# Kernel tuning notes

Measured on AMD Instinct MI355X. Metric: run time of the kernel, lower is better.

Reference implementation:

```python
import jax, jax.numpy as jnp
import numpy as np
from jax import lax

NB_DIGITS = 2
BASE = 10
NUMS = BASE ** NB_DIGITS            # 100 possible values per number
SUMS = 2 * (NUMS - 1) + 1           # 199 possible sums (circuit roots)
B = 4096                            # logical batch size
N_IMAGES = B * 2 * NB_DIGITS        # 16384 digit images


def setup_inputs() -> dict:
    key = jax.random.key(0)
    ks = jax.random.split(key, 11)
    s = 0.1
    return {
        "images": jax.random.normal(ks[0], (N_IMAGES, 1, 28, 28), jnp.float32),
        "conv1_w": jax.random.normal(ks[1], (6, 1, 5, 5), jnp.float32) * s,
        "conv1_b": jax.random.normal(ks[2], (6,), jnp.float32) * s,
        "conv2_w": jax.random.normal(ks[3], (16, 6, 5, 5), jnp.float32) * s,
        "conv2_b": jax.random.normal(ks[4], (16,), jnp.float32) * s,
        "fc1_w": jax.random.normal(ks[5], (120, 256), jnp.float32) * s,
        "fc1_b": jax.random.normal(ks[6], (120,), jnp.float32) * s,
        "fc2_w": jax.random.normal(ks[7], (84, 120), jnp.float32) * s,
        "fc2_b": jax.random.normal(ks[8], (84,), jnp.float32) * s,
        "fc3_w": jax.random.normal(ks[9], (10, 84), jnp.float32) * s,
        "fc3_b": jax.random.normal(ks[10], (10,), jnp.float32) * s,
    }


def _conv(x, w, b):
    y = lax.conv_general_dilated(x, w, (1, 1), 'VALID',
                                 dimension_numbers=('NCHW', 'OIHW', 'NCHW'))
    return y + b[None, :, None, None]


def _maxpool2(x):
    return lax.reduce_window(x, -jnp.inf, lax.max, (1, 1, 2, 2), (1, 1, 2, 2), 'VALID')


def _lenet(x, c1w, c1b, c2w, c2b, f1w, f1b, f2w, f2b, f3w, f3b):
    x = jax.nn.relu(_maxpool2(_conv(x, c1w, c1b)))   # [N,6,12,12]
    x = jax.nn.relu(_maxpool2(_conv(x, c2w, c2b)))   # [N,16,4,4]
    x = x.reshape(-1, 16 * 4 * 4)
    x = jax.nn.relu(x @ f1w.T + f1b)
    x = jax.nn.relu(x @ f2w.T + f2b)
    x = x @ f3w.T + f3b
    return jax.nn.log_softmax(x, axis=-1)            # [N,10]


def _circuit(lp):
    # lp: [B, 2*NB_DIGITS, 10] per-digit log-probs.
    # Vars layout from get_circuit: positions 0..NB_DIGITS-1 = n1 digits (MSB first),
    # positions NB_DIGITS..2*NB_DIGITS-1 = n2 digits. Neg-literal weights are 0 in
    # log space (the `zeros` arg), so each model's weight = sum of digit log-probs;
    # OR over models = logsumexp grouped by n1+n2.
    d = jnp.arange(NUMS)
    hi, lo = d // BASE, d % BASE
    lp1 = lp[:, 0, hi] + lp[:, 1, lo]                # [B, NUMS] log P(n1=k)
    lp2 = lp[:, 2, hi] + lp[:, 3, lo]                # [B, NUMS] log P(n2=k)
    M = (lp1[:, :, None] + lp2[:, None, :]).reshape(lp.shape[0], -1)  # [B, NUMS^2]
    seg = (jnp.arange(NUMS)[:, None] + jnp.arange(NUMS)[None, :]).reshape(-1)
    Mf = M.T                                          # [NUMS^2, B]
    m = jax.ops.segment_max(Mf, seg, num_segments=SUMS)              # [SUMS, B]
    ssum = jax.ops.segment_sum(jnp.exp(Mf - m[seg]), seg, num_segments=SUMS)
    return (jnp.log(ssum) + m).T                      # [B, SUMS] log P(sum=s)


def reference(images, conv1_w, conv1_b, conv2_w, conv2_b,
              fc1_w, fc1_b, fc2_w, fc2_b, fc3_w, fc3_b):
    logp = _lenet(images, conv1_w, conv1_b, conv2_w, conv2_b,
                  fc1_w, fc1_b, fc2_w, fc2_b, fc3_w, fc3_b)   # [N_IMAGES,10]
    lp = logp.reshape(B, 2 * NB_DIGITS, BASE)
    return _circuit(lp)
```

## Files before the change

### kernel.cpp

```cpp
#include <hip/hip_runtime.h>
#include <hip/hip_bf16.h>
#include <math.h>

#define SUMS 199
#define NBLK 1024

typedef __attribute__((ext_vector_type(8))) short short8;
typedef __attribute__((ext_vector_type(4))) float float4v;

union Frag8 { short8 v; unsigned u[4]; uint4 q; };

static __device__ inline unsigned pk_bf16(float a, float b) {
    __hip_bfloat162 h = __float22bfloat162_rn(make_float2(a, b));
    union { __hip_bfloat162 h; unsigned u; } c; c.h = h; return c.u;
}

__global__ __launch_bounds__(256) void convert_weights(
    const float* __restrict__ f1w, const float* __restrict__ f2w,
    const float* __restrict__ f3w, const float* __restrict__ c1w,
    const float* __restrict__ c2w, uint4* __restrict__ ws)
{
    const int g = blockIdx.x * 256 + threadIdx.x;
    if (g >= 6400) return;
    float v[8];
    if (g < 5824) {
        const float* W; int O, K, ld, nt, s, l;
        if (g < 4096)      { W = f1w; O = 120; K = 256; ld = 256; nt = g >> 9; s = (g >> 6) & 7; l = g & 63; }
        else if (g < 5632) { const int f = g - 4096; W = f2w; O = 84; K = 120; ld = 120; nt = f >> 8; s = (f >> 6) & 3; l = f & 63; }
        else               { const int f = g - 5632; W = f3w; O = 10; K = 84;  ld = 84;  nt = 0; s = f >> 6; l = f & 63; }
        const int o = nt * 16 + (l & 15);
        #pragma unroll
        for (int j = 0; j < 8; ++j) {
            const int k = 32 * s + 8 * (l >> 4) + j;
            v[j] = (o < O && k < K) ? W[o * ld + k] : 0.f;
        }
    } else if (g < 6336) {
        const int f = g - 5824, s = f >> 6, l = f & 63;
        const int c = l & 15, h = l >> 4;
        #pragma unroll
        for (int jp = 0; jp < 4; ++jp) {
            const int D = 16 * s + 4 * h + jp;
            const int ky = D / 24, rem = D % 24, kx = rem >> 2, icp = rem & 3;
            const bool ok = (ky < 5 && kx < 5);
            v[2 * jp]     = (ok && 2 * icp < 6)     ? c2w[c * 150 + (2 * icp) * 25 + ky * 5 + kx]     : 0.f;
            v[2 * jp + 1] = (ok && 2 * icp + 1 < 6) ? c2w[c * 150 + (2 * icp + 1) * 25 + ky * 5 + kx] : 0.f;
        }
    } else {
        const int l = (g - 6336) & 63;
        const int c = l & 15, h = l >> 4;
        const int oc = c >> 1, xs = c & 1;
        #pragma unroll
        for (int j = 0; j < 8; ++j) {
            const int p = h * 4 + (j >> 1);
            float w = 0.f;
            if (p < 15 && c < 12) {
                const int ky = p / 3, kx = 2 * (p % 3) + (j & 1) - xs;
                if (kx >= 0 && kx < 5) w = c1w[oc * 25 + ky * 5 + kx];
            }
            v[j] = w;
        }
    }
    uint4 r;
    r.x = pk_bf16(v[0], v[1]); r.y = pk_bf16(v[2], v[3]);
    r.z = pk_bf16(v[4], v[5]); r.w = pk_bf16(v[6], v[7]);
    ws[g] = r;
}

__global__ __launch_bounds__(256) void lenet_circuit_kernel(
    const float* __restrict__ images,
    const float* __restrict__ c1b, const float* __restrict__ c2b,
    const float* __restrict__ f1b, const float* __restrict__ f2b,
    const float* __restrict__ f3b, const uint4* __restrict__ wsb,
    float* __restrict__ out)
{
    __shared__ __align__(16) unsigned char s_mem[39712];
    unsigned*       imgu = (unsigned*)s_mem;
    unsigned short* p1s  = (unsigned short*)(s_mem + 12576);
    const uint4*    p1u4 = (const uint4*)(s_mem + 12576);
    unsigned*       A1d  = (unsigned*)(s_mem + 31264);
    const uint4*    A1q  = (const uint4*)(s_mem + 31264);

    const int t = threadIdx.x, bid = blockIdx.x;
    const int lane = t & 63, wav = t >> 6;
    const int c = lane & 15, h = lane >> 4;
    const uint4 z4 = {0u, 0u, 0u, 0u};

    {
        uint4* pz = (uint4*)(s_mem + 12576);
        for (int i = t; i < 1168; i += 256) pz[i] = z4;
    }
    Frag8 a1; a1.q = wsb[6336 + lane];
    Frag8 w2[8];
    #pragma unroll
    for (int s = 0; s < 8; ++s) w2[s].q = wsb[5824 + s * 64 + lane];
    int koff[8];
    #pragma unroll
    for (int s = 0; s < 8; ++s) {
        const int D0 = 16 * s + 4 * h;
        koff[s] = (D0 / 24) * 12 + ((D0 % 24) >> 2);
    }
    int pd[4];
    #pragma unroll
    for (int q = 0; q < 4; ++q) {
        const int p = 4 * h + q;
        pd[q] = (p < 15) ? (p / 3) * 14 + (p % 3) : 0;
    }
    float bias0 = 0.f, bias1 = 0.f;
    if (h < 3) { bias0 = c1b[2 * h]; bias1 = c1b[2 * h + 1]; }
    const float b2v = c2b[c];

    for (int pass = 0; pass < 2; ++pass) {
        {
            const float4* g = (const float4*)(images + (size_t)bid * 12544 + pass * 6272);
            for (int i = t; i < 1568; i += 256) {
                const float4 v = g[i];
                const int im = i / 196, j = i % 196;
                imgu[im * 393 + 2 * j]     = pk_bf16(v.x, v.y);
                imgu[im * 393 + 2 * j + 1] = pk_bf16(v.z, v.w);
            }
        }
        __syncthreads();

        {
            const int n = c, img = n >> 1;
            const int imb = img * 393 + (n & 1) * 14;
            for (int qy = wav * 3; qy < wav * 3 + 3; ++qy) {
                #pragma unroll
                for (int qx = 0; qx < 12; ++qx) {
                    const int base = imb + qy * 28 + qx;
                    Frag8 bf;
                    #pragma unroll
                    for (int q = 0; q < 4; ++q) bf.u[q] = imgu[base + pd[q]];
                    float4v acc = {0.f, 0.f, 0.f, 0.f};
                    acc = __builtin_amdgcn_mfma_f32_16x16x32_bf16(a1.v, bf.v, acc, 0, 0, 0);
                    float v0 = fmaxf(acc[0], acc[1]);
                    float v1 = fmaxf(acc[2], acc[3]);
                    v0 = fmaxf(v0, __shfl_xor(v0, 1));
                    v1 = fmaxf(v1, __shfl_xor(v1, 1));
                    if ((n & 1) == 0 && h < 3) {
                        const unsigned pkv = pk_bf16(fmaxf(v0 + bias0, 0.f),
                                                     fmaxf(v1 + bias1, 0.f));
                        *(unsigned*)&p1s[img * 1152 + qy * 96 + qx * 8 + 2 * h] = pkv;
                    }
                }
            }
        }
        __syncthreads();

        {
            const int pxl = (c & 1) + 2 * ((c >> 2) & 1);
            const int pyl = ((c >> 1) & 1) + 2 * ((c >> 3) & 1);
            #pragma unroll
            for (int ii = 0; ii < 2; ++ii) {
                const int i0 = 2 * wav + ii;
                #pragma unroll
                for (int mt = 0; mt < 4; ++mt) {
                    const int px = pxl + 4 * (mt & 1), py = pyl + 4 * (mt >> 1);
                    const int base = i0 * 144 + py * 12 + px;
                    float4v acc = {0.f, 0.f, 0.f, 0.f};
                    #pragma unroll
                    for (int s = 0; s < 8; ++s) {
                        Frag8 af; af.q = p1u4[base + koff[s]];
                        acc = __builtin_amdgcn_mfma_f32_16x16x32_bf16(af.v, w2[s].v, acc, 0, 0, 0);
                    }
                    const float p = fmaxf(fmaxf(acc[0], acc[1]), fmaxf(acc[2], acc[3]));
                    float v = fmaxf(p + b2v, 0.f);
                    const float vp = __shfl_xor(v, 16);
                    if ((h & 1) == 0) {
                        const int qy = (h >> 1) + 2 * (mt >> 1);
                        A1d[(pass * 8 + i0) * 132 + c * 8 + qy * 2 + (mt & 1)] = pk_bf16(v, vp);
                    }
                }
            }
        }
    }
    __syncthreads();

    {
        unsigned* A2d = (unsigned*)s_mem;
        if (t < 64) A2d[(t >> 2) * 68 + 60 + (t & 3)] = 0u;
        float4v acc0 = {0.f, 0.f, 0.f, 0.f}, acc1 = acc0;
        const int nt0 = 2 * wav;
        #pragma unroll
        for (int s = 0; s < 8; ++s) {
            Frag8 af; af.q = A1q[c * 33 + 4 * s + h];
            Frag8 b0; b0.q = wsb[(nt0 * 8 + s) * 64 + lane];
            Frag8 b1; b1.q = wsb[((nt0 + 1) * 8 + s) * 64 + lane];
            acc0 = __builtin_amdgcn_mfma_f32_16x16x32_bf16(af.v, b0.v, acc0, 0, 0, 0);
            acc1 = __builtin_amdgcn_mfma_f32_16x16x32_bf16(af.v, b1.v, acc1, 0, 0, 0);
        }
        #pragma unroll
        for (int ntl = 0; ntl < 2; ++ntl) {
            const int o = 32 * wav + 16 * ntl + c;
            const float bias = (o < 120) ? f1b[o] : 0.f;
            #pragma unroll
            for (int r = 0; r < 4; ++r) {
                float v = fmaxf((ntl ? acc1[r] : acc0[r]) + bias, 0.f);
                const float vp = __shfl_xor(v, 1);
                if ((c & 1) == 0 && o < 120)
                    A2d[(4 * h + r) * 68 + (o >> 1)] = pk_bf16(v, vp);
            }
        }
    }
    __syncthreads();

    {
        unsigned* A3d = (unsigned*)(s_mem + 4352);
        if (t < 96) A3d[(t / 6) * 52 + 42 + (t % 6)] = 0u;
        if (wav < 3) {
            const uint4* A2q = (const uint4*)s_mem;
            float4v acc0 = {0.f, 0.f, 0.f, 0.f}, acc1 = acc0;
            const int nt0 = 2 * wav;
            #pragma unroll
            for (int s = 0; s < 4; ++s) {
                Frag8 af; af.q = A2q[c * 17 + 4 * s + h];
                Frag8 b0; b0.q = wsb[4096 + (nt0 * 4 + s) * 64 + lane];
                Frag8 b1; b1.q = wsb[4096 + ((nt0 + 1) * 4 + s) * 64 + lane];
                acc0 = __builtin_amdgcn_mfma_f32_16x16x32_bf16(af.v, b0.v, acc0, 0, 0, 0);
                acc1 = __builtin_amdgcn_mfma_f32_16x16x32_bf16(af.v, b1.v, acc1, 0, 0, 0);
            }
            #pragma unroll
            for (int ntl = 0; ntl < 2; ++ntl) {
                const int o = 32 * wav + 16 * ntl + c;
                const float bias = (o < 84) ? f2b[o] : 0.f;
                #pragma unroll
                for (int r = 0; r < 4; ++r) {
                    float v = fmaxf((ntl ? acc1[r] : acc0[r]) + bias, 0.f);
                    const float vp = __shfl_xor(v, 1);
                    if ((c & 1) == 0 && o < 84)
                        A3d[(4 * h + r) * 52 + (o >> 1)] = pk_bf16(v, vp);
                }
            }
        }
    }
    __syncthreads();

    float* lgf = (float*)(s_mem + 7680);
    float* e1f = (float*)(s_mem + 8448);
    float* e2f = (float*)(s_mem + 10048);

    if (wav == 0) {
        const uint4* A3q = (const uint4*)(s_mem + 4352);
        float4v acc = {0.f, 0.f, 0.f, 0.f};
        #pragma unroll
        for (int s = 0; s < 3; ++s) {
            Frag8 af; af.q = A3q[c * 13 + 4 * s + h];
            Frag8 b; b.q = wsb[5632 + s * 64 + lane];
            acc = __builtin_amdgcn_mfma_f32_16x16x32_bf16(af.v, b.v, acc, 0, 0, 0);
        }
        if (c < 10) {
            const float bias = f3b[c];
            #pragma unroll
            for (int r = 0; r < 4; ++r) lgf[(4 * h + r) * 12 + c] = acc[r] + bias;
        }
    }
    __syncthreads();

    if (t < 16) {
        float* lp = lgf + t * 12;
        float mx = -INFINITY;
        #pragma unroll
        for (int i = 0; i < 10; ++i) mx = fmaxf(mx, lp[i]);
        float sum = 0.f;
        #pragma unroll
        for (int i = 0; i < 10; ++i) sum += expf(lp[i] - mx);
        const float lse = mx + logf(sum);
        #pragma unroll
        for (int i = 0; i < 10; ++i) lp[i] -= lse;
    }
    __syncthreads();

    for (int idx = t; idx < 800; idx += 256) {
        const int be = idx / 200, r = idx % 200;
        const float* lp = lgf + 4 * be * 12;
        if (r < 100) e1f[be * 100 + r] = expf(lp[r / 10] + lp[12 + r % 10]);
        else { const int k = r - 100; e2f[be * 100 + k] = expf(lp[24 + k / 10] + lp[36 + k % 10]); }
    }
    __syncthreads();

    for (int pid = t; pid < 400; pid += 256) {
        const int be = pid / 100, sp = pid % 100;
        const float* E1 = e1f + be * 100;
        const float* E2 = e2f + be * 100;
        float* ob = out + ((size_t)bid * 4 + be) * SUMS;
        float s1 = 0.f;
        for (int i = 0; i <= sp; ++i) s1 += E1[i] * E2[sp - i];
        ob[sp] = logf(s1);
        if (sp >= 1) {
            float s2 = 0.f;
            for (int i = sp; i <= 99; ++i) s2 += E1[i] * E2[sp + 99 - i];
            ob[sp + 99] = logf(s2);
        }
    }
}

extern "C" void kernel_launch(void* const* d_in, const int* in_sizes, int n_in,
                              void* d_out, int out_size, void* d_ws, size_t ws_size,
                              hipStream_t stream) {
    const float* images = (const float*)d_in[0];
    const float* c1w = (const float*)d_in[1];
    const float* c1b = (const float*)d_in[2];
    const float* c2w = (const float*)d_in[3];
    const float* c2b = (const float*)d_in[4];
    const float* f1w = (const float*)d_in[5];
    const float* f1b = (const float*)d_in[6];
    const float* f2w = (const float*)d_in[7];
    const float* f2b = (const float*)d_in[8];
    const float* f3w = (const float*)d_in[9];
    const float* f3b = (const float*)d_in[10];
    float* out = (float*)d_out;

    convert_weights<<<25, 256, 0, stream>>>(f1w, f2w, f3w, c1w, c2w, (uint4*)d_ws);
    lenet_circuit_kernel<<<NBLK, 256, 0, stream>>>(
        images, c1b, c2b, f1b, f2b, f3b, (const uint4*)d_ws, out);
}
```

Before: 151.4 us.

## Double block to 512 threads and vectorize circuit convolution with phase-shifted float4 buffers

The fused kernel now launches 512 threads (8 waves) per block, and every stage's work split is redistributed so each wave handles fewer conv tiles, images or FC output tiles. The final sum-convolution stores zero-padded, phase-shifted copies of E1 and a reversed E2 so each output is a contiguous aligned float4 dot product. One thread now computes each output pair, so more threads do work at once and the shared-memory loads are vectorized. The cost is higher register pressure from launch_bounds(512,8), more LDS writes for the four phase copies, and some idle waves in the FC3 stage.

Result: slower. 260.0 us (+71.8%).

```diff
diff --git a/kernel.cpp b/kernel.cpp
--- a/kernel.cpp
+++ b/kernel.cpp
@@ -66,7 +66,7 @@
     ws[g] = r;
 }
 
-__global__ __launch_bounds__(256) void lenet_circuit_kernel(
+__global__ __launch_bounds__(512, 8) void lenet_circuit_kernel(
     const float* __restrict__ images,
     const float* __restrict__ c1b, const float* __restrict__ c2b,
     const float* __restrict__ f1b, const float* __restrict__ f2b,
@@ -79,6 +79,8 @@
     const uint4*    p1u4 = (const uint4*)(s_mem + 12576);
     unsigned*       A1d  = (unsigned*)(s_mem + 31264);
     const uint4*    A1q  = (const uint4*)(s_mem + 31264);
+    float*          E1Pf = (float*)(s_mem + 12576);
+    float*          E2Rf = (float*)(s_mem + 19232);
 
     const int t = threadIdx.x, bid = blockIdx.x;
     const int lane = t & 63, wav = t >> 6;
@@ -87,7 +89,7 @@
 
     {
         uint4* pz = (uint4*)(s_mem + 12576);
-        for (int i = t; i < 1168; i += 256) pz[i] = z4;
+        for (int i = t; i < 1168; i += 512) pz[i] = z4;
     }
     Frag8 a1; a1.q = wsb[6336 + lane];
     Frag8 w2[8];
@@ -112,7 +114,7 @@
     for (int pass = 0; pass < 2; ++pass) {
         {
             const float4* g = (const float4*)(images + (size_t)bid * 12544 + pass * 6272);
-            for (int i = t; i < 1568; i += 256) {
+            for (int i = t; i < 1568; i += 512) {
                 const float4 v = g[i];
                 const int im = i / 196, j = i % 196;
                 imgu[im * 393 + 2 * j]     = pk_bf16(v.x, v.y);
@@ -124,82 +126,73 @@
         {
             const int n = c, img = n >> 1;
             const int imb = img * 393 + (n & 1) * 14;
-            for (int qy = wav * 3; qy < wav * 3 + 3; ++qy) {
+            for (int task = wav * 18; task < wav * 18 + 18; ++task) {
+                const int qy = task / 12, qx = task % 12;
+                const int base = imb + qy * 28 + qx;
+                Frag8 bf;
                 #pragma unroll
-                for (int qx = 0; qx < 12; ++qx) {
-                    const int base = imb + qy * 28 + qx;
-                    Frag8 bf;
-                    #pragma unroll
-                    for (int q = 0; q < 4; ++q) bf.u[q] = imgu[base + pd[q]];
-                    float4v acc = {0.f, 0.f, 0.f, 0.f};
-                    acc = __builtin_amdgcn_mfma_f32_16x16x32_bf16(a1.v, bf.v, acc, 0, 0, 0);
-                    float v0 = fmaxf(acc[0], acc[1]);
-                    float v1 = fmaxf(acc[2], acc[3]);
-                    v0 = fmaxf(v0, __shfl_xor(v0, 1));
-                    v1 = fmaxf(v1, __shfl_xor(v1, 1));
-                    if ((n & 1) == 0 && h < 3) {
-                        const unsigned pkv = pk_bf16(fmaxf(v0 + bias0, 0.f),
-                                                     fmaxf(v1 + bias1, 0.f));
-                        *(unsigned*)&p1s[img * 1152 + qy * 96 + qx * 8 + 2 * h] = pkv;
-                    }
+                for (int q = 0; q < 4; ++q) bf.u[q] = imgu[base + pd[q]];
+                float4v acc = {0.f, 0.f, 0.f, 0.f};
+                acc = __builtin_amdgcn_mfma_f32_16x16x32_bf16(a1.v, bf.v, acc, 0, 0, 0);
+                float v0 = fmaxf(acc[0], acc[1]);
+                float v1 = fmaxf(acc[2], acc[3]);
+                v0 = fmaxf(v0, __shfl_xor(v0, 1));
+                v1 = fmaxf(v1, __shfl_xor(v1, 1));
+                if ((n & 1) == 0 && h < 3) {
+                    const unsigned pkv = pk_bf16(fmaxf(v0 + bias0, 0.f),
+                                                 fmaxf(v1 + bias1, 0.f));
+                    *(unsigned*)&p1s[img * 1152 + qy * 96 + qx * 8 + 2 * h] = pkv;
                 }
             }
         }
         __syncthreads();
 
         {
+            const int i0 = wav;
             const int pxl = (c & 1) + 2 * ((c >> 2) & 1);
             const int pyl = ((c >> 1) & 1) + 2 * ((c >> 3) & 1);
             #pragma unroll
-            for (int ii = 0; ii < 2; ++ii) {
-                const int i0 = 2 * wav + ii;
+            for (int mt = 0; mt < 4; ++mt) {
+                const int px = pxl + 4 * (mt & 1), py = pyl + 4 * (mt >> 1);
+                const int base = i0 * 144 + py * 12 + px;
+                float4v acc = {0.f, 0.f, 0.f, 0.f};
                 #pragma unroll
-                for (int mt = 0; mt < 4; ++mt) {
-                    const int px = pxl + 4 * (mt & 1), py = pyl + 4 * (mt >> 1);
-                    const int base = i0 * 144 + py * 12 + px;
-                    float4v acc = {0.f, 0.f, 0.f, 0.f};
-                    #pragma unroll
-                    for (int s = 0; s < 8; ++s) {
-                        Frag8 af; af.q = p1u4[base + koff[s]];
-                        acc = __builtin_amdgcn_mfma_f32_16x16x32_bf16(af.v, w2[s].v, acc, 0, 0, 0);
-                    }
-                    const float p = fmaxf(fmaxf(acc[0], acc[1]), fmaxf(acc[2], acc[3]));
-                    float v = fmaxf(p + b2v, 0.f);
-                    const float vp = __shfl_xor(v, 16);
-                    if ((h & 1) == 0) {
-                        const int qy = (h >> 1) + 2 * (mt >> 1);
-                        A1d[(pass * 8 + i0) * 132 + c * 8 + qy * 2 + (mt & 1)] = pk_bf16(v, vp);
-                    }
+                for (int s = 0; s < 8; ++s) {
+                    Frag8 af; af.q = p1u4[base + koff[s]];
+                    acc = __builtin_amdgcn_mfma_f32_16x16x32_bf16(af.v, w2[s].v, acc, 0, 0, 0);
                 }
+                const float p = fmaxf(fmaxf(acc[0], acc[1]), fmaxf(acc[2], acc[3]));
+                float v = fmaxf(p + b2v, 0.f);
+                const float vp = __shfl_xor(v, 16);
+                if ((h & 1) == 0) {
+                    const int qy = (h >> 1) + 2 * (mt >> 1);
+                    A1d[(pass * 8 + i0) * 132 + c * 8 + qy * 2 + (mt & 1)] = pk_bf16(v, vp);
+                }
             }
         }
     }
     __syncthreads();
 
     {
+        uint4* pz = (uint4*)(s_mem + 12576);
+        for (int i = t; i < 832; i += 512) pz[i] = z4;
         unsigned* A2d = (unsigned*)s_mem;
         if (t < 64) A2d[(t >> 2) * 68 + 60 + (t & 3)] = 0u;
-        float4v acc0 = {0.f, 0.f, 0.f, 0.f}, acc1 = acc0;
-        const int nt0 = 2 * wav;
+        float4v acc = {0.f, 0.f, 0.f, 0.f};
         #pragma unroll
         for (int s = 0; s < 8; ++s) {
             Frag8 af; af.q = A1q[c * 33 + 4 * s + h];
-            Frag8 b0; b0.q = wsb[(nt0 * 8 + s) * 64 + lane];
-            Frag8 b1; b1.q = wsb[((nt0 + 1) * 8 + s) * 64 + lane];
-            acc0 = __builtin_amdgcn_mfma_f32_16x16x32_bf16(af.v, b0.v, acc0, 0, 0, 0);
-            acc1 = __builtin_amdgcn_mfma_f32_16x16x32_bf16(af.v, b1.v, acc1, 0, 0, 0);
-        }
-        #pragma unroll
-        for (int ntl = 0; ntl < 2; ++ntl) {
-            const int o = 32 * wav + 16 * ntl + c;
-            const float bias = (o < 120) ? f1b[o] : 0.f;
-            #pragma unroll
-            for (int r = 0; r < 4; ++r) {
-                float v = fmaxf((ntl ? acc1[r] : acc0[r]) + bias, 0.f);
-                const float vp = __shfl_xor(v, 1);
-                if ((c & 1) == 0 && o < 120)
-                    A2d[(4 * h + r) * 68 + (o >> 1)] = pk_bf16(v, vp);
-            }
+            Frag8 b; b.q = wsb[(wav * 8 + s) * 64 + lane];
+            acc = __builtin_amdgcn_mfma_f32_16x16x32_bf16(af.v, b.v, acc, 0, 0, 0);
+        }
+        const int o = 16 * wav + c;
+        const float bias = (o < 120) ? f1b[o] : 0.f;
+        #pragma unroll
+        for (int r = 0; r < 4; ++r) {
+            float v = fmaxf(acc[r] + bias, 0.f);
+            const float vp = __shfl_xor(v, 1);
+            if ((c & 1) == 0 && o < 120)
+                A2d[(4 * h + r) * 68 + (o >> 1)] = pk_bf16(v, vp);
         }
     }
     __syncthreads();
@@ -207,37 +200,29 @@
     {
         unsigned* A3d = (unsigned*)(s_mem + 4352);
         if (t < 96) A3d[(t / 6) * 52 + 42 + (t % 6)] = 0u;
-        if (wav < 3) {
+        if (wav < 6) {
             const uint4* A2q = (const uint4*)s_mem;
-            float4v acc0 = {0.f, 0.f, 0.f, 0.f}, acc1 = acc0;
-            const int nt0 = 2 * wav;
+            float4v acc = {0.f, 0.f, 0.f, 0.f};
             #pragma unroll
             for (int s = 0; s < 4; ++s) {
                 Frag8 af; af.q = A2q[c * 17 + 4 * s + h];
-                Frag8 b0; b0.q = wsb[4096 + (nt0 * 4 + s) * 64 + lane];
-                Frag8 b1; b1.q = wsb[4096 + ((nt0 + 1) * 4 + s) * 64 + lane];
-                acc0 = __builtin_amdgcn_mfma_f32_16x16x32_bf16(af.v, b0.v, acc0, 0, 0, 0);
-                acc1 = __builtin_amdgcn_mfma_f32_16x16x32_bf16(af.v, b1.v, acc1, 0, 0, 0);
-            }
-            #pragma unroll
-            for (int ntl = 0; ntl < 2; ++ntl) {
-                const int o = 32 * wav + 16 * ntl + c;
-                const float bias = (o < 84) ? f2b[o] : 0.f;
-                #pragma unroll
-                for (int r = 0; r < 4; ++r) {
-                    float v = fmaxf((ntl ? acc1[r] : acc0[r]) + bias, 0.f);
-                    const float vp = __shfl_xor(v, 1);
-                    if ((c & 1) == 0 && o < 84)
-                        A3d[(4 * h + r) * 52 + (o >> 1)] = pk_bf16(v, vp);
-                }
+                Frag8 b; b.q = wsb[4096 + (wav * 4 + s) * 64 + lane];
+                acc = __builtin_amdgcn_mfma_f32_16x16x32_bf16(af.v, b.v, acc, 0, 0, 0);
+            }
+            const int o = 16 * wav + c;
+            const float bias = (o < 84) ? f2b[o] : 0.f;
+            #pragma unroll
+            for (int r = 0; r < 4; ++r) {
+                float v = fmaxf(acc[r] + bias, 0.f);
+                const float vp = __shfl_xor(v, 1);
+                if ((c & 1) == 0 && o < 84)
+                    A3d[(4 * h + r) * 52 + (o >> 1)] = pk_bf16(v, vp);
             }
         }
     }
     __syncthreads();
 
     float* lgf = (float*)(s_mem + 7680);
-    float* e1f = (float*)(s_mem + 8448);
-    float* e2f = (float*)(s_mem + 10048);
 
     if (wav == 0) {
         const uint4* A3q = (const uint4*)(s_mem + 4352);
@@ -270,26 +255,43 @@
     }
     __syncthreads();
 
-    for (int idx = t; idx < 800; idx += 256) {
+    for (int idx = t; idx < 800; idx += 512) {
         const int be = idx / 200, r = idx % 200;
         const float* lp = lgf + 4 * be * 12;
-        if (r < 100) e1f[be * 100 + r] = expf(lp[r / 10] + lp[12 + r % 10]);
-        else { const int k = r - 100; e2f[be * 100 + k] = expf(lp[24 + k / 10] + lp[36 + k % 10]); }
-    }
-    __syncthreads();
-
-    for (int pid = t; pid < 400; pid += 256) {
-        const int be = pid / 100, sp = pid % 100;
-        const float* E1 = e1f + be * 100;
-        const float* E2 = e2f + be * 100;
+        if (r < 100) {
+            const float v = expf(lp[r / 10] + lp[12 + r % 10]);
+            #pragma unroll
+            for (int ph = 0; ph < 4; ++ph)
+                E1Pf[(ph * 4 + be) * 104 + r + ph] = v;
+        } else {
+            const int k = r - 100;
+            const float v = expf(lp[24 + k / 10] + lp[36 + k % 10]);
+            #pragma unroll
+            for (int ph = 0; ph < 4; ++ph)
+                E2Rf[(ph * 4 + be) * 104 + (99 - k) + ph] = v;
+        }
+    }
+    __syncthreads();
+
+    if (t < 400) {
+        const int be = t / 100, sp = t % 100;
         float* ob = out + ((size_t)bid * 4 + be) * SUMS;
-        float s1 = 0.f;
-        for (int i = 0; i <= sp; ++i) s1 += E1[i] * E2[sp - i];
-        ob[sp] = logf(s1);
-        if (sp >= 1) {
-            float s2 = 0.f;
-            for (int i = sp; i <= 99; ++i) s2 += E1[i] * E2[sp + 99 - i];
-            ob[sp + 99] = logf(s2);
+        #pragma unroll
+        for (int form = 0; form < 2; ++form) {
+            const int o1 = form ? sp : 0;
+            const int o2 = form ? 0 : 99 - sp;
+            const int len = form ? 100 - sp : sp + 1;
+            if (form && sp == 0) break;
+            const int ph1 = (4 - (o1 & 3)) & 3, ph2 = (4 - (o2 & 3)) & 3;
+            const float4* P1 = (const float4*)(E1Pf + (ph1 * 4 + be) * 104) + ((o1 + ph1) >> 2);
+            const float4* P2 = (const float4*)(E2Rf + (ph2 * 4 + be) * 104) + ((o2 + ph2) >> 2);
+            const int nv = (len + 3) >> 2;
+            float s = 0.f;
+            for (int j = 0; j < nv; ++j) {
+                const float4 a = P1[j], b = P2[j];
+                s += a.x * b.x + a.y * b.y + a.z * b.z + a.w * b.w;
+            }
+            ob[form ? sp + 99 : sp] = logf(s);
         }
     }
 }
@@ -311,6 +313,6 @@
     float* out = (float*)d_out;
 
     convert_weights<<<25, 256, 0, stream>>>(f1w, f2w, f3w, c1w, c2w, (uint4*)d_ws);
-    lenet_circuit_kernel<<<NBLK, 256, 0, stream>>>(
+    lenet_circuit_kernel<<<NBLK, 512, 0, stream>>>(
         images, c1b, c2b, f1b, f2b, f3b, (const uint4*)d_ws, out);
 }
```

## Fuse log-softmax into fc3 wave via shuffles and vectorize circuit convolution

Applied to the files above, without the earlier changes.

Computes log-softmax directly in the fc3 wave with cross-lane shuffle reductions, removing a separate 16-thread pass and one barrier. Stores the exponentiated marginals as four phase-shifted, zero-padded copies, with the second one reversed, so every anti-diagonal convolution sum can be read as aligned float4 vectors. Padding with zeros lets the vector loops run past the true length without affecting the result. This costs extra shared-memory writes and a zeroing pass over the region.

Measured after the change: 146.2 us. -3.4%, faster.

```diff
diff --git a/kernel.cpp b/kernel.cpp
--- a/kernel.cpp
+++ b/kernel.cpp
@@ -79,6 +79,8 @@
     const uint4*    p1u4 = (const uint4*)(s_mem + 12576);
     unsigned*       A1d  = (unsigned*)(s_mem + 31264);
     const uint4*    A1q  = (const uint4*)(s_mem + 31264);
+    float*          E1Pf = (float*)(s_mem + 12576);
+    float*          E2Rf = (float*)(s_mem + 19232);
 
     const int t = threadIdx.x, bid = blockIdx.x;
     const int lane = t & 63, wav = t >> 6;
@@ -177,6 +179,8 @@
     __syncthreads();
 
     {
+        uint4* pz = (uint4*)(s_mem + 12576);
+        for (int i = t; i < 832; i += 256) pz[i] = z4;
         unsigned* A2d = (unsigned*)s_mem;
         if (t < 64) A2d[(t >> 2) * 68 + 60 + (t & 3)] = 0u;
         float4v acc0 = {0.f, 0.f, 0.f, 0.f}, acc1 = acc0;
@@ -236,8 +240,6 @@
     __syncthreads();
 
     float* lgf = (float*)(s_mem + 7680);
-    float* e1f = (float*)(s_mem + 8448);
-    float* e2f = (float*)(s_mem + 10048);
 
     if (wav == 0) {
         const uint4* A3q = (const uint4*)(s_mem + 4352);
@@ -248,48 +250,68 @@
             Frag8 b; b.q = wsb[5632 + s * 64 + lane];
             acc = __builtin_amdgcn_mfma_f32_16x16x32_bf16(af.v, b.v, acc, 0, 0, 0);
         }
+        const float bias = (c < 10) ? f3b[c] : 0.f;
+        float x[4], m[4], sm[4];
+        #pragma unroll
+        for (int r = 0; r < 4; ++r) {
+            x[r] = (c < 10) ? (acc[r] + bias) : -INFINITY;
+            m[r] = x[r];
+        }
+        #pragma unroll
+        for (int d = 1; d <= 8; d <<= 1)
+            #pragma unroll
+            for (int r = 0; r < 4; ++r) m[r] = fmaxf(m[r], __shfl_xor(m[r], d));
+        #pragma unroll
+        for (int r = 0; r < 4; ++r) sm[r] = (c < 10) ? expf(x[r] - m[r]) : 0.f;
+        #pragma unroll
+        for (int d = 1; d <= 8; d <<= 1)
+            #pragma unroll
+            for (int r = 0; r < 4; ++r) sm[r] += __shfl_xor(sm[r], d);
         if (c < 10) {
-            const float bias = f3b[c];
-            #pragma unroll
-            for (int r = 0; r < 4; ++r) lgf[(4 * h + r) * 12 + c] = acc[r] + bias;
-        }
-    }
-    __syncthreads();
-
-    if (t < 16) {
-        float* lp = lgf + t * 12;
-        float mx = -INFINITY;
-        #pragma unroll
-        for (int i = 0; i < 10; ++i) mx = fmaxf(mx, lp[i]);
-        float sum = 0.f;
-        #pragma unroll
-        for (int i = 0; i < 10; ++i) sum += expf(lp[i] - mx);
-        const float lse = mx + logf(sum);
-        #pragma unroll
-        for (int i = 0; i < 10; ++i) lp[i] -= lse;
+            #pragma unroll
+            for (int r = 0; r < 4; ++r)
+                lgf[(4 * h + r) * 12 + c] = x[r] - (m[r] + logf(sm[r]));
+        }
     }
     __syncthreads();
 
     for (int idx = t; idx < 800; idx += 256) {
         const int be = idx / 200, r = idx % 200;
         const float* lp = lgf + 4 * be * 12;
-        if (r < 100) e1f[be * 100 + r] = expf(lp[r / 10] + lp[12 + r % 10]);
-        else { const int k = r - 100; e2f[be * 100 + k] = expf(lp[24 + k / 10] + lp[36 + k % 10]); }
+        if (r < 100) {
+            const float v = expf(lp[r / 10] + lp[12 + r % 10]);
+            #pragma unroll
+            for (int ph = 0; ph < 4; ++ph)
+                E1Pf[(ph * 4 + be) * 104 + r + ph] = v;
+        } else {
+            const int k = r - 100;
+            const float v = expf(lp[24 + k / 10] + lp[36 + k % 10]);
+            #pragma unroll
+            for (int ph = 0; ph < 4; ++ph)
+                E2Rf[(ph * 4 + be) * 104 + (99 - k) + ph] = v;
+        }
     }
     __syncthreads();
 
     for (int pid = t; pid < 400; pid += 256) {
         const int be = pid / 100, sp = pid % 100;
-        const float* E1 = e1f + be * 100;
-        const float* E2 = e2f + be * 100;
         float* ob = out + ((size_t)bid * 4 + be) * SUMS;
-        float s1 = 0.f;
-        for (int i = 0; i <= sp; ++i) s1 += E1[i] * E2[sp - i];
-        ob[sp] = logf(s1);
-        if (sp >= 1) {
-            float s2 = 0.f;
-            for (int i = sp; i <= 99; ++i) s2 += E1[i] * E2[sp + 99 - i];
-            ob[sp + 99] = logf(s2);
+        #pragma unroll
+        for (int form = 0; form < 2; ++form) {
+            const int o1 = form ? sp : 0;
+            const int o2 = form ? 0 : 99 - sp;
+            const int len = form ? 100 - sp : sp + 1;
+            if (form && sp == 0) break;
+            const int ph1 = (4 - (o1 & 3)) & 3, ph2 = (4 - (o2 & 3)) & 3;
+            const float4* P1 = (const float4*)(E1Pf + (ph1 * 4 + be) * 104) + ((o1 + ph1) >> 2);
+            const float4* P2 = (const float4*)(E2Rf + (ph2 * 4 + be) * 104) + ((o2 + ph2) >> 2);
+            const int nv = (len + 3) >> 2;
+            float s = 0.f;
+            for (int j = 0; j < nv; ++j) {
+                const float4 a = P1[j], b = P2[j];
+                s += a.x * b.x + a.y * b.y + a.z * b.z + a.w * b.w;
+            }
+            ob[form ? sp + 99 : sp] = logf(s);
         }
     }
 }
```
